# Kernel optimization log

Hardware: AMD Instinct MI355X
Metric: run time of the kernel (lower is better)

The kernel has to match this reference:

```python
import jax, jax.numpy as jnp
import numpy as np

N = 100000
E = 640000
D_IN = 128
D_OUT = 128
EPS = 0.0


def setup_inputs() -> dict:
    key = jax.random.key(0)
    k1, k2, k3, k4, k5, k6 = jax.random.split(key, 6)
    x = jax.random.normal(k1, (N, D_IN), dtype=jnp.float32)
    edge_index = jax.random.randint(k2, (2, E), 0, N, dtype=jnp.int64)
    # MLP params (Linear(in,out) -> ReLU -> Linear(out,out)), PyTorch-style init scale
    s1 = 1.0 / np.sqrt(D_IN)
    s2 = 1.0 / np.sqrt(D_OUT)
    W1 = jax.random.uniform(k3, (D_IN, D_OUT), minval=-s1, maxval=s1, dtype=jnp.float32)
    b1 = jax.random.uniform(k4, (D_OUT,), minval=-s1, maxval=s1, dtype=jnp.float32)
    W2 = jax.random.uniform(k5, (D_OUT, D_OUT), minval=-s2, maxval=s2, dtype=jnp.float32)
    b2 = jax.random.uniform(k6, (D_OUT,), minval=-s2, maxval=s2, dtype=jnp.float32)
    return {"x": x, "edge_index": edge_index, "W1": W1, "b1": b1, "W2": W2, "b2": b2}


def reference(x, edge_index, W1, b1, W2, b2):
    row, col = edge_index[0], edge_index[1]
    # gather source features, scatter-add into destination nodes
    aggregated = jax.ops.segment_sum(x[row], col, num_segments=N)  # [N, D_IN]
    h = (1.0 + EPS) * x + aggregated
    h = jnp.maximum(h @ W1 + b1, 0.0)
    return h @ W2 + b2
```

## Files before the change

kernel.cpp:

```cpp
#include <hip/hip_runtime.h>

#define NN 100000
#define EE 640000
#define DD 128

#define CVT_BLKS  12500
#define PREP_BLKS 128
#define ZERO_BLKS 98

typedef short bf16x8 __attribute__((ext_vector_type(8)));
typedef float f32x4 __attribute__((ext_vector_type(4)));

__device__ __forceinline__ unsigned short f2bf(float f) {
    union { float f; unsigned int u; } a; a.f = f;
    unsigned int u = a.u + 0x7fffu + ((a.u >> 16) & 1u);
    return (unsigned short)(u >> 16);
}

__device__ __forceinline__ int wave_incl_scan(int v, int lane) {
#pragma unroll
    for (int d = 1; d < 64; d <<= 1) {
        int u = __shfl_up(v, d, 64);
        if (lane >= d) v += u;
    }
    return v;
}

__global__ __launch_bounds__(256) void k_setup(const float* __restrict__ x,
                                               const float* __restrict__ W1,
                                               const float* __restrict__ W2,
                                               unsigned short* __restrict__ xb,
                                               unsigned short* __restrict__ w1t,
                                               unsigned short* __restrict__ w2t,
                                               int* __restrict__ cnt) {
    int b = blockIdx.x, t = threadIdx.x;
    if (b < CVT_BLKS) {
        int i = (b * 256 + t) * 4;
        float4 v = *reinterpret_cast<const float4*>(x + i);
        unsigned int u0 = (unsigned)f2bf(v.x) | ((unsigned)f2bf(v.y) << 16);
        unsigned int u1 = (unsigned)f2bf(v.z) | ((unsigned)f2bf(v.w) << 16);
        *reinterpret_cast<uint2*>(xb + i) = make_uint2(u0, u1);
    } else if (b < CVT_BLKS + PREP_BLKS) {
        int idx = (b - CVT_BLKS) * 256 + t;
        const float* W = (idx < DD * DD) ? W1 : W2;
        unsigned short* O = (idx < DD * DD) ? w1t : w2t;
        int i = idx & (DD * DD - 1);
        int n = i >> 7, k = i & (DD - 1);
        O[i] = f2bf(W[k * DD + n]);
    } else {
        int idx = (b - CVT_BLKS - PREP_BLKS) * 256 + t;
        if (idx < 25001)
            reinterpret_cast<int4*>(cnt)[idx] = make_int4(0, 0, 0, 0);
    }
}

__global__ __launch_bounds__(256) void k_hist(const int* __restrict__ ei,
                                              int* __restrict__ cnt) {
    int e = blockIdx.x * 256 + threadIdx.x;
    if (e >= EE) return;
    atomicAdd(&cnt[ei[EE + e]], 1);
}

__global__ __launch_bounds__(256) void k_offs(int* __restrict__ cnt,
                                              int* __restrict__ offs,
                                              int* __restrict__ gcount) {
    int t = threadIdx.x, lane = t & 63, w = t >> 6;
    int i = blockIdx.x * 256 + t;
    int v = (i < NN) ? cnt[i] : 0;
    int s = wave_incl_scan(v, lane);
    __shared__ int wsum[4];
    __shared__ int base;
    if (lane == 63) wsum[w] = s;
    __syncthreads();
    if (t == 0)
        base = atomicAdd(gcount, wsum[0] + wsum[1] + wsum[2] + wsum[3]);
    __syncthreads();
    int off = base;
    for (int k = 0; k < w; ++k) off += wsum[k];
    int start = off + s - v;
    if (i < NN) { offs[i] = start; cnt[i] = start; }
}

__global__ __launch_bounds__(256) void k_fill(const int* __restrict__ ei,
                                              int* __restrict__ cnt,
                                              int* __restrict__ bucket) {
    int e = blockIdx.x * 256 + threadIdx.x;
    if (e >= EE) return;
    int r = ei[e];
    int c = ei[EE + e];
    int p = atomicAdd(&cnt[c], 1);
    bucket[p] = r;
}

__global__ __launch_bounds__(256) void k_gather(const unsigned int* __restrict__ xr,
                                                const int* __restrict__ offs,
                                                const int* __restrict__ cnt,
                                                const int* __restrict__ bucket,
                                                unsigned int* __restrict__ hb) {
    int gid = blockIdx.x * 256 + threadIdx.x;
    int n = gid >> 6;
    if (n >= NN) return;
    int l = gid & 63;
    unsigned int u = xr[(size_t)n * 64 + l];
    float ax = __uint_as_float(u << 16);
    float ay = __uint_as_float(u & 0xffff0000u);
    int j = offs[n], je = cnt[n];
    for (; j + 7 < je; j += 8) {
        int a0 = bucket[j],     a1 = bucket[j + 1], a2 = bucket[j + 2], a3 = bucket[j + 3];
        int a4 = bucket[j + 4], a5 = bucket[j + 5], a6 = bucket[j + 6], a7 = bucket[j + 7];
        unsigned int u0 = xr[(size_t)a0 * 64 + l];
        unsigned int u1 = xr[(size_t)a1 * 64 + l];
        unsigned int u2 = xr[(size_t)a2 * 64 + l];
        unsigned int u3 = xr[(size_t)a3 * 64 + l];
        unsigned int u4 = xr[(size_t)a4 * 64 + l];
        unsigned int u5 = xr[(size_t)a5 * 64 + l];
        unsigned int u6 = xr[(size_t)a6 * 64 + l];
        unsigned int u7 = xr[(size_t)a7 * 64 + l];
        ax += __uint_as_float(u0 << 16) + __uint_as_float(u1 << 16)
            + __uint_as_float(u2 << 16) + __uint_as_float(u3 << 16)
            + __uint_as_float(u4 << 16) + __uint_as_float(u5 << 16)
            + __uint_as_float(u6 << 16) + __uint_as_float(u7 << 16);
        ay += __uint_as_float(u0 & 0xffff0000u) + __uint_as_float(u1 & 0xffff0000u)
            + __uint_as_float(u2 & 0xffff0000u) + __uint_as_float(u3 & 0xffff0000u)
            + __uint_as_float(u4 & 0xffff0000u) + __uint_as_float(u5 & 0xffff0000u)
            + __uint_as_float(u6 & 0xffff0000u) + __uint_as_float(u7 & 0xffff0000u);
    }
    if (j + 3 < je) {
        int a0 = bucket[j], a1 = bucket[j + 1], a2 = bucket[j + 2], a3 = bucket[j + 3];
        unsigned int u0 = xr[(size_t)a0 * 64 + l];
        unsigned int u1 = xr[(size_t)a1 * 64 + l];
        unsigned int u2 = xr[(size_t)a2 * 64 + l];
        unsigned int u3 = xr[(size_t)a3 * 64 + l];
        ax += __uint_as_float(u0 << 16) + __uint_as_float(u1 << 16)
            + __uint_as_float(u2 << 16) + __uint_as_float(u3 << 16);
        ay += __uint_as_float(u0 & 0xffff0000u) + __uint_as_float(u1 & 0xffff0000u)
            + __uint_as_float(u2 & 0xffff0000u) + __uint_as_float(u3 & 0xffff0000u);
        j += 4;
    }
    for (; j < je; ++j) {
        unsigned int uu = xr[(size_t)bucket[j] * 64 + l];
        ax += __uint_as_float(uu << 16);
        ay += __uint_as_float(uu & 0xffff0000u);
    }
    hb[(size_t)n * 64 + l] = (unsigned)f2bf(ax) | ((unsigned)f2bf(ay) << 16);
}

__global__ __launch_bounds__(256, 2) void k_mlp(const unsigned short* __restrict__ hb,
                                                const unsigned short* __restrict__ w1t,
                                                const unsigned short* __restrict__ w2t,
                                                const float* __restrict__ b1,
                                                const float* __restrict__ b2,
                                                float* __restrict__ out) {
    __shared__ unsigned short lds[DD * DD];
    const int t  = threadIdx.x;
    const int w  = t >> 6, l = t & 63;
    const int wr = w >> 1, wc = w & 1;
    const int hi = l >> 4, lo = l & 15;
    const long base_row = (long)blockIdx.x * 128;

    const uint4* hrow = reinterpret_cast<const uint4*>(hb);
#pragma unroll
    for (int it = 0; it < 8; ++it) {
        int idx = it * 256 + t;
        int row = idx >> 4;
        long g = base_row + row;
        uint4 v = make_uint4(0u, 0u, 0u, 0u);
        if (g < NN) v = hrow[base_row * 16 + idx];
        int byte = (row * 256 + (idx & 15) * 16) ^ ((row & 7) << 4);
        *reinterpret_cast<uint4*>(reinterpret_cast<char*>(lds) + byte) = v;
    }
    __syncthreads();

    const f32x4 zero = {0.f, 0.f, 0.f, 0.f};

    bf16x8 bw1[4][4];
#pragma unroll
    for (int n = 0; n < 4; ++n)
#pragma unroll
        for (int k = 0; k < 4; ++k)
            bw1[n][k] = *reinterpret_cast<const bf16x8*>(
                w1t + (wc * 64 + n * 16 + lo) * DD + k * 32 + hi * 8);

    f32x4 acc[4][4];
#pragma unroll
    for (int m = 0; m < 4; ++m)
#pragma unroll
        for (int n = 0; n < 4; ++n) acc[m][n] = zero;
#pragma unroll
    for (int m = 0; m < 4; ++m) {
        bf16x8 a[4];
        int r = wr * 64 + m * 16 + lo;
#pragma unroll
        for (int k = 0; k < 4; ++k) {
            int byte = (r * 256 + k * 64 + hi * 16) ^ ((r & 7) << 4);
            a[k] = *reinterpret_cast<const bf16x8*>(reinterpret_cast<const char*>(lds) + byte);
        }
#pragma unroll
        for (int n = 0; n < 4; ++n)
#pragma unroll
            for (int k = 0; k < 4; ++k)
                acc[m][n] = __builtin_amdgcn_mfma_f32_16x16x32_bf16(a[k], bw1[n][k], acc[m][n], 0, 0, 0);
    }
    __syncthreads();

    float bias1[4];
#pragma unroll
    for (int n = 0; n < 4; ++n) bias1[n] = b1[wc * 64 + n * 16 + lo];
#pragma unroll
    for (int m = 0; m < 4; ++m)
#pragma unroll
        for (int n = 0; n < 4; ++n)
#pragma unroll
            for (int g = 0; g < 4; ++g) {
                int row = wr * 64 + m * 16 + hi * 4 + g;
                int col = wc * 64 + n * 16 + lo;
                float v = fmaxf(acc[m][n][g] + bias1[n], 0.f);
                int byte = (row * 256 + col * 2) ^ ((row & 7) << 4);
                *reinterpret_cast<unsigned short*>(reinterpret_cast<char*>(lds) + byte) = f2bf(v);
            }
    __syncthreads();

    bf16x8 bw2[4][4];
#pragma unroll
    for (int n = 0; n < 4; ++n)
#pragma unroll
        for (int k = 0; k < 4; ++k)
            bw2[n][k] = *reinterpret_cast<const bf16x8*>(
                w2t + (wc * 64 + n * 16 + lo) * DD + k * 32 + hi * 8);

    f32x4 acc2[4][4];
#pragma unroll
    for (int m = 0; m < 4; ++m)
#pragma unroll
        for (int n = 0; n < 4; ++n) acc2[m][n] = zero;
#pragma unroll
    for (int m = 0; m < 4; ++m) {
        bf16x8 a[4];
        int r = wr * 64 + m * 16 + lo;
#pragma unroll
        for (int k = 0; k < 4; ++k) {
            int byte = (r * 256 + k * 64 + hi * 16) ^ ((r & 7) << 4);
            a[k] = *reinterpret_cast<const bf16x8*>(reinterpret_cast<const char*>(lds) + byte);
        }
#pragma unroll
        for (int n = 0; n < 4; ++n)
#pragma unroll
            for (int k = 0; k < 4; ++k)
                acc2[m][n] = __builtin_amdgcn_mfma_f32_16x16x32_bf16(a[k], bw2[n][k], acc2[m][n], 0, 0, 0);
    }

    float bias2[4];
#pragma unroll
    for (int n = 0; n < 4; ++n) bias2[n] = b2[wc * 64 + n * 16 + lo];
#pragma unroll
    for (int m = 0; m < 4; ++m)
#pragma unroll
        for (int n = 0; n < 4; ++n)
#pragma unroll
            for (int g = 0; g < 4; ++g) {
                long row = base_row + wr * 64 + m * 16 + hi * 4 + g;
                if (row < NN)
                    out[row * DD + wc * 64 + n * 16 + lo] = acc2[m][n][g] + bias2[n];
            }
}

extern "C" void kernel_launch(void* const* d_in, const int* in_sizes, int n_in,
                              void* d_out, int out_size, void* d_ws, size_t ws_size,
                              hipStream_t stream) {
    const float* x  = (const float*)d_in[0];
    const int*   ei = (const int*)d_in[1];
    const float* W1 = (const float*)d_in[2];
    const float* b1 = (const float*)d_in[3];
    const float* W2 = (const float*)d_in[4];
    const float* b2 = (const float*)d_in[5];
    float* out = (float*)d_out;

    char* ws = (char*)d_ws;
    unsigned short* xb  = (unsigned short*)ws;
    unsigned short* w1t = (unsigned short*)(ws + 25600000);
    unsigned short* w2t = w1t + DD * DD;
    unsigned short* hb  = (unsigned short*)(ws + 25665536);
    int* cnt    = (int*)(ws + 51265536);
    int* offs   = cnt + NN + 4;
    int* bucket = offs + NN + 4;

    k_setup<<<CVT_BLKS + PREP_BLKS + ZERO_BLKS, 256, 0, stream>>>(x, W1, W2, xb, w1t, w2t, cnt);
    k_hist<<<(EE + 255) / 256, 256, 0, stream>>>(ei, cnt);
    k_offs<<<(NN + 255) / 256, 256, 0, stream>>>(cnt, offs, cnt + NN);
    k_fill<<<(EE + 255) / 256, 256, 0, stream>>>(ei, cnt, bucket);
    k_gather<<<(NN * 64 + 255) / 256, 256, 0, stream>>>(
        (const unsigned int*)xb, offs, cnt, bucket, (unsigned int*)hb);
    k_mlp<<<(NN + 127) / 128, 256, 0, stream>>>(hb, w1t, w2t, b1, b2, out);
}
```

Measured before the change: 253.5 us.

## Fuse all stages into one persistent cooperative kernel with grid syncs

Replaces six separate kernel launches with a single cooperative persistent kernel that runs zeroing, histogram, conversion, scan, bucket fill, gather and MLP as phases separated by grid.sync. Grid-stride loops replace per-stage grids, and the host queries occupancy and CU count to size the grid. The aim is to remove launch gaps between the small stages. In exchange, every phase runs at the register and LDS occupancy of the heaviest MFMA phase, and grid-wide barriers add their own cost.

Measured after the change: 660.0 us. +160.3%, slower.

```diff
diff --git a/kernel.cpp b/kernel.cpp
--- a/kernel.cpp
+++ b/kernel.cpp
@@ -1,12 +1,11 @@
 #include <hip/hip_runtime.h>
+#include <hip/hip_cooperative_groups.h>
+
+namespace cg = cooperative_groups;
 
 #define NN 100000
 #define EE 640000
 #define DD 128
-
-#define CVT_BLKS  12500
-#define PREP_BLKS 128
-#define ZERO_BLKS 98
 
 typedef short bf16x8 __attribute__((ext_vector_type(8)));
 typedef float f32x4 __attribute__((ext_vector_type(4)));
@@ -26,242 +25,236 @@
     return v;
 }
 
-__global__ __launch_bounds__(256) void k_setup(const float* __restrict__ x,
-                                               const float* __restrict__ W1,
-                                               const float* __restrict__ W2,
-                                               unsigned short* __restrict__ xb,
-                                               unsigned short* __restrict__ w1t,
-                                               unsigned short* __restrict__ w2t,
-                                               int* __restrict__ cnt) {
-    int b = blockIdx.x, t = threadIdx.x;
-    if (b < CVT_BLKS) {
-        int i = (b * 256 + t) * 4;
-        float4 v = *reinterpret_cast<const float4*>(x + i);
+__global__ __launch_bounds__(256, 4) void k_mega(
+    const float* __restrict__ x, const int* __restrict__ ei,
+    const float* __restrict__ W1, const float* __restrict__ b1,
+    const float* __restrict__ W2, const float* __restrict__ b2,
+    float* __restrict__ out,
+    unsigned short* __restrict__ xb, unsigned short* __restrict__ w1t,
+    unsigned short* __restrict__ w2t, unsigned short* __restrict__ hb,
+    int* __restrict__ cnt, int* __restrict__ offs, int* __restrict__ bucket)
+{
+    cg::grid_group grid = cg::this_grid();
+    const int t = threadIdx.x;
+    const int bid = blockIdx.x;
+    const int nb = gridDim.x;
+    const int gthreads = nb * 256;
+    const int gt = bid * 256 + t;
+    const int lane = t & 63, wv = t >> 6;
+
+    __shared__ unsigned short lds[DD * DD];
+    __shared__ int wsum[4];
+    __shared__ int base;
+
+    for (int i = gt; i < (NN + 4) / 4; i += gthreads)
+        reinterpret_cast<int4*>(cnt)[i] = make_int4(0, 0, 0, 0);
+    grid.sync();
+
+    for (int e = gt; e < EE; e += gthreads)
+        atomicAdd(&cnt[ei[EE + e]], 1);
+    for (int i = gt; i < NN * DD / 4; i += gthreads) {
+        float4 v = *reinterpret_cast<const float4*>(x + (size_t)i * 4);
         unsigned int u0 = (unsigned)f2bf(v.x) | ((unsigned)f2bf(v.y) << 16);
         unsigned int u1 = (unsigned)f2bf(v.z) | ((unsigned)f2bf(v.w) << 16);
-        *reinterpret_cast<uint2*>(xb + i) = make_uint2(u0, u1);
-    } else if (b < CVT_BLKS + PREP_BLKS) {
-        int idx = (b - CVT_BLKS) * 256 + t;
+        *reinterpret_cast<uint2*>(xb + (size_t)i * 4) = make_uint2(u0, u1);
+    }
+    for (int idx = gt; idx < 2 * DD * DD; idx += gthreads) {
         const float* W = (idx < DD * DD) ? W1 : W2;
         unsigned short* O = (idx < DD * DD) ? w1t : w2t;
         int i = idx & (DD * DD - 1);
         int n = i >> 7, k = i & (DD - 1);
         O[i] = f2bf(W[k * DD + n]);
-    } else {
-        int idx = (b - CVT_BLKS - PREP_BLKS) * 256 + t;
-        if (idx < 25001)
-            reinterpret_cast<int4*>(cnt)[idx] = make_int4(0, 0, 0, 0);
-    }
-}
-
-__global__ __launch_bounds__(256) void k_hist(const int* __restrict__ ei,
-                                              int* __restrict__ cnt) {
-    int e = blockIdx.x * 256 + threadIdx.x;
-    if (e >= EE) return;
-    atomicAdd(&cnt[ei[EE + e]], 1);
-}
-
-__global__ __launch_bounds__(256) void k_offs(int* __restrict__ cnt,
-                                              int* __restrict__ offs,
-                                              int* __restrict__ gcount) {
-    int t = threadIdx.x, lane = t & 63, w = t >> 6;
-    int i = blockIdx.x * 256 + t;
-    int v = (i < NN) ? cnt[i] : 0;
-    int s = wave_incl_scan(v, lane);
-    __shared__ int wsum[4];
-    __shared__ int base;
-    if (lane == 63) wsum[w] = s;
-    __syncthreads();
-    if (t == 0)
-        base = atomicAdd(gcount, wsum[0] + wsum[1] + wsum[2] + wsum[3]);
-    __syncthreads();
-    int off = base;
-    for (int k = 0; k < w; ++k) off += wsum[k];
-    int start = off + s - v;
-    if (i < NN) { offs[i] = start; cnt[i] = start; }
-}
-
-__global__ __launch_bounds__(256) void k_fill(const int* __restrict__ ei,
-                                              int* __restrict__ cnt,
-                                              int* __restrict__ bucket) {
-    int e = blockIdx.x * 256 + threadIdx.x;
-    if (e >= EE) return;
-    int r = ei[e];
-    int c = ei[EE + e];
-    int p = atomicAdd(&cnt[c], 1);
-    bucket[p] = r;
-}
-
-__global__ __launch_bounds__(256) void k_gather(const unsigned int* __restrict__ xr,
-                                                const int* __restrict__ offs,
-                                                const int* __restrict__ cnt,
-                                                const int* __restrict__ bucket,
-                                                unsigned int* __restrict__ hb) {
-    int gid = blockIdx.x * 256 + threadIdx.x;
-    int n = gid >> 6;
-    if (n >= NN) return;
-    int l = gid & 63;
-    unsigned int u = xr[(size_t)n * 64 + l];
-    float ax = __uint_as_float(u << 16);
-    float ay = __uint_as_float(u & 0xffff0000u);
-    int j = offs[n], je = cnt[n];
-    for (; j + 7 < je; j += 8) {
-        int a0 = bucket[j],     a1 = bucket[j + 1], a2 = bucket[j + 2], a3 = bucket[j + 3];
-        int a4 = bucket[j + 4], a5 = bucket[j + 5], a6 = bucket[j + 6], a7 = bucket[j + 7];
-        unsigned int u0 = xr[(size_t)a0 * 64 + l];
-        unsigned int u1 = xr[(size_t)a1 * 64 + l];
-        unsigned int u2 = xr[(size_t)a2 * 64 + l];
-        unsigned int u3 = xr[(size_t)a3 * 64 + l];
-        unsigned int u4 = xr[(size_t)a4 * 64 + l];
-        unsigned int u5 = xr[(size_t)a5 * 64 + l];
-        unsigned int u6 = xr[(size_t)a6 * 64 + l];
-        unsigned int u7 = xr[(size_t)a7 * 64 + l];
-        ax += __uint_as_float(u0 << 16) + __uint_as_float(u1 << 16)
-            + __uint_as_float(u2 << 16) + __uint_as_float(u3 << 16)
-            + __uint_as_float(u4 << 16) + __uint_as_float(u5 << 16)
-            + __uint_as_float(u6 << 16) + __uint_as_float(u7 << 16);
-        ay += __uint_as_float(u0 & 0xffff0000u) + __uint_as_float(u1 & 0xffff0000u)
-            + __uint_as_float(u2 & 0xffff0000u) + __uint_as_float(u3 & 0xffff0000u)
-            + __uint_as_float(u4 & 0xffff0000u) + __uint_as_float(u5 & 0xffff0000u)
-            + __uint_as_float(u6 & 0xffff0000u) + __uint_as_float(u7 & 0xffff0000u);
-    }
-    if (j + 3 < je) {
-        int a0 = bucket[j], a1 = bucket[j + 1], a2 = bucket[j + 2], a3 = bucket[j + 3];
-        unsigned int u0 = xr[(size_t)a0 * 64 + l];
-        unsigned int u1 = xr[(size_t)a1 * 64 + l];
-        unsigned int u2 = xr[(size_t)a2 * 64 + l];
-        unsigned int u3 = xr[(size_t)a3 * 64 + l];
-        ax += __uint_as_float(u0 << 16) + __uint_as_float(u1 << 16)
-            + __uint_as_float(u2 << 16) + __uint_as_float(u3 << 16);
-        ay += __uint_as_float(u0 & 0xffff0000u) + __uint_as_float(u1 & 0xffff0000u)
-            + __uint_as_float(u2 & 0xffff0000u) + __uint_as_float(u3 & 0xffff0000u);
-        j += 4;
-    }
-    for (; j < je; ++j) {
-        unsigned int uu = xr[(size_t)bucket[j] * 64 + l];
-        ax += __uint_as_float(uu << 16);
-        ay += __uint_as_float(uu & 0xffff0000u);
-    }
-    hb[(size_t)n * 64 + l] = (unsigned)f2bf(ax) | ((unsigned)f2bf(ay) << 16);
-}
-
-__global__ __launch_bounds__(256, 2) void k_mlp(const unsigned short* __restrict__ hb,
-                                                const unsigned short* __restrict__ w1t,
-                                                const unsigned short* __restrict__ w2t,
-                                                const float* __restrict__ b1,
-                                                const float* __restrict__ b2,
-                                                float* __restrict__ out) {
-    __shared__ unsigned short lds[DD * DD];
-    const int t  = threadIdx.x;
-    const int w  = t >> 6, l = t & 63;
-    const int wr = w >> 1, wc = w & 1;
-    const int hi = l >> 4, lo = l & 15;
-    const long base_row = (long)blockIdx.x * 128;
-
-    const uint4* hrow = reinterpret_cast<const uint4*>(hb);
-#pragma unroll
-    for (int it = 0; it < 8; ++it) {
-        int idx = it * 256 + t;
-        int row = idx >> 4;
-        long g = base_row + row;
-        uint4 v = make_uint4(0u, 0u, 0u, 0u);
-        if (g < NN) v = hrow[base_row * 16 + idx];
-        int byte = (row * 256 + (idx & 15) * 16) ^ ((row & 7) << 4);
-        *reinterpret_cast<uint4*>(reinterpret_cast<char*>(lds) + byte) = v;
-    }
-    __syncthreads();
-
-    const f32x4 zero = {0.f, 0.f, 0.f, 0.f};
-
-    bf16x8 bw1[4][4];
-#pragma unroll
-    for (int n = 0; n < 4; ++n)
-#pragma unroll
-        for (int k = 0; k < 4; ++k)
-            bw1[n][k] = *reinterpret_cast<const bf16x8*>(
-                w1t + (wc * 64 + n * 16 + lo) * DD + k * 32 + hi * 8);
-
-    f32x4 acc[4][4];
-#pragma unroll
-    for (int m = 0; m < 4; ++m)
-#pragma unroll
-        for (int n = 0; n < 4; ++n) acc[m][n] = zero;
-#pragma unroll
-    for (int m = 0; m < 4; ++m) {
-        bf16x8 a[4];
-        int r = wr * 64 + m * 16 + lo;
-#pragma unroll
-        for (int k = 0; k < 4; ++k) {
-            int byte = (r * 256 + k * 64 + hi * 16) ^ ((r & 7) << 4);
-            a[k] = *reinterpret_cast<const bf16x8*>(reinterpret_cast<const char*>(lds) + byte);
+    }
+    grid.sync();
+
+    for (int tile = bid; tile < (NN + 255) / 256; tile += nb) {
+        int i = tile * 256 + t;
+        int v = (i < NN) ? cnt[i] : 0;
+        int s = wave_incl_scan(v, lane);
+        if (lane == 63) wsum[wv] = s;
+        __syncthreads();
+        if (t == 0)
+            base = atomicAdd(&cnt[NN], wsum[0] + wsum[1] + wsum[2] + wsum[3]);
+        __syncthreads();
+        int off = base;
+        for (int k = 0; k < wv; ++k) off += wsum[k];
+        int start = off + s - v;
+        if (i < NN) { offs[i] = start; cnt[i] = start; }
+        __syncthreads();
+    }
+    grid.sync();
+
+    for (int e = gt; e < EE; e += gthreads) {
+        int r = ei[e];
+        int c = ei[EE + e];
+        bucket[atomicAdd(&cnt[c], 1)] = r;
+    }
+    grid.sync();
+
+    {
+        const unsigned int* xr = reinterpret_cast<const unsigned int*>(xb);
+        unsigned int* hbw = reinterpret_cast<unsigned int*>(hb);
+        int gw = bid * 4 + wv, nw = nb * 4;
+        for (int n = gw; n < NN; n += nw) {
+            unsigned int u = xr[(size_t)n * 64 + lane];
+            float ax = __uint_as_float(u << 16);
+            float ay = __uint_as_float(u & 0xffff0000u);
+            int j = offs[n], je = cnt[n];
+            for (; j + 7 < je; j += 8) {
+                int a0 = bucket[j],     a1 = bucket[j + 1], a2 = bucket[j + 2], a3 = bucket[j + 3];
+                int a4 = bucket[j + 4], a5 = bucket[j + 5], a6 = bucket[j + 6], a7 = bucket[j + 7];
+                unsigned int u0 = xr[(size_t)a0 * 64 + lane];
+                unsigned int u1 = xr[(size_t)a1 * 64 + lane];
+                unsigned int u2 = xr[(size_t)a2 * 64 + lane];
+                unsigned int u3 = xr[(size_t)a3 * 64 + lane];
+                unsigned int u4 = xr[(size_t)a4 * 64 + lane];
+                unsigned int u5 = xr[(size_t)a5 * 64 + lane];
+                unsigned int u6 = xr[(size_t)a6 * 64 + lane];
+                unsigned int u7 = xr[(size_t)a7 * 64 + lane];
+                ax += __uint_as_float(u0 << 16) + __uint_as_float(u1 << 16)
+                    + __uint_as_float(u2 << 16) + __uint_as_float(u3 << 16)
+                    + __uint_as_float(u4 << 16) + __uint_as_float(u5 << 16)
+                    + __uint_as_float(u6 << 16) + __uint_as_float(u7 << 16);
+                ay += __uint_as_float(u0 & 0xffff0000u) + __uint_as_float(u1 & 0xffff0000u)
+                    + __uint_as_float(u2 & 0xffff0000u) + __uint_as_float(u3 & 0xffff0000u)
+                    + __uint_as_float(u4 & 0xffff0000u) + __uint_as_float(u5 & 0xffff0000u)
+                    + __uint_as_float(u6 & 0xffff0000u) + __uint_as_float(u7 & 0xffff0000u);
+            }
+            if (j + 3 < je) {
+                int a0 = bucket[j], a1 = bucket[j + 1], a2 = bucket[j + 2], a3 = bucket[j + 3];
+                unsigned int u0 = xr[(size_t)a0 * 64 + lane];
+                unsigned int u1 = xr[(size_t)a1 * 64 + lane];
+                unsigned int u2 = xr[(size_t)a2 * 64 + lane];
+                unsigned int u3 = xr[(size_t)a3 * 64 + lane];
+                ax += __uint_as_float(u0 << 16) + __uint_as_float(u1 << 16)
+                    + __uint_as_float(u2 << 16) + __uint_as_float(u3 << 16);
+                ay += __uint_as_float(u0 & 0xffff0000u) + __uint_as_float(u1 & 0xffff0000u)
+                    + __uint_as_float(u2 & 0xffff0000u) + __uint_as_float(u3 & 0xffff0000u);
+                j += 4;
+            }
+            for (; j < je; ++j) {
+                unsigned int uu = xr[(size_t)bucket[j] * 64 + lane];
+                ax += __uint_as_float(uu << 16);
+                ay += __uint_as_float(uu & 0xffff0000u);
+            }
+            hbw[(size_t)n * 64 + lane] = (unsigned)f2bf(ax) | ((unsigned)f2bf(ay) << 16);
         }
-#pragma unroll
-        for (int n = 0; n < 4; ++n)
-#pragma unroll
-            for (int k = 0; k < 4; ++k)
-                acc[m][n] = __builtin_amdgcn_mfma_f32_16x16x32_bf16(a[k], bw1[n][k], acc[m][n], 0, 0, 0);
-    }
-    __syncthreads();
-
-    float bias1[4];
-#pragma unroll
-    for (int n = 0; n < 4; ++n) bias1[n] = b1[wc * 64 + n * 16 + lo];
-#pragma unroll
-    for (int m = 0; m < 4; ++m)
-#pragma unroll
-        for (int n = 0; n < 4; ++n)
-#pragma unroll
-            for (int g = 0; g < 4; ++g) {
-                int row = wr * 64 + m * 16 + hi * 4 + g;
-                int col = wc * 64 + n * 16 + lo;
-                float v = fmaxf(acc[m][n][g] + bias1[n], 0.f);
-                int byte = (row * 256 + col * 2) ^ ((row & 7) << 4);
-                *reinterpret_cast<unsigned short*>(reinterpret_cast<char*>(lds) + byte) = f2bf(v);
-            }
-    __syncthreads();
-
-    bf16x8 bw2[4][4];
-#pragma unroll
-    for (int n = 0; n < 4; ++n)
-#pragma unroll
-        for (int k = 0; k < 4; ++k)
-            bw2[n][k] = *reinterpret_cast<const bf16x8*>(
-                w2t + (wc * 64 + n * 16 + lo) * DD + k * 32 + hi * 8);
-
-    f32x4 acc2[4][4];
-#pragma unroll
-    for (int m = 0; m < 4; ++m)
-#pragma unroll
-        for (int n = 0; n < 4; ++n) acc2[m][n] = zero;
-#pragma unroll
-    for (int m = 0; m < 4; ++m) {
-        bf16x8 a[4];
-        int r = wr * 64 + m * 16 + lo;
-#pragma unroll
-        for (int k = 0; k < 4; ++k) {
-            int byte = (r * 256 + k * 64 + hi * 16) ^ ((r & 7) << 4);
-            a[k] = *reinterpret_cast<const bf16x8*>(reinterpret_cast<const char*>(lds) + byte);
+    }
+    grid.sync();
+
+    {
+        const int wr = wv >> 1, wc = wv & 1;
+        const int hi = lane >> 4, lo = lane & 15;
+        const f32x4 zero = {0.f, 0.f, 0.f, 0.f};
+        const uint4* hrow = reinterpret_cast<const uint4*>(hb);
+
+        for (int tile = bid; tile < (NN + 127) / 128; tile += nb) {
+            const long base_row = (long)tile * 128;
+
+#pragma unroll
+            for (int it = 0; it < 8; ++it) {
+                int idx = it * 256 + t;
+                int row = idx >> 4;
+                long g = base_row + row;
+                uint4 v = make_uint4(0u, 0u, 0u, 0u);
+                if (g < NN) v = hrow[base_row * 16 + idx];
+                int byte = (row * 256 + (idx & 15) * 16) ^ ((row & 7) << 4);
+                *reinterpret_cast<uint4*>(reinterpret_cast<char*>(lds) + byte) = v;
+            }
+            __syncthreads();
+
+            bf16x8 bw1[4][4];
+#pragma unroll
+            for (int n = 0; n < 4; ++n)
+#pragma unroll
+                for (int k = 0; k < 4; ++k)
+                    bw1[n][k] = *reinterpret_cast<const bf16x8*>(
+                        w1t + (wc * 64 + n * 16 + lo) * DD + k * 32 + hi * 8);
+
+            f32x4 acc[4][4];
+#pragma unroll
+            for (int m = 0; m < 4; ++m)
+#pragma unroll
+                for (int n = 0; n < 4; ++n) acc[m][n] = zero;
+#pragma unroll
+            for (int m = 0; m < 4; ++m) {
+                bf16x8 a[4];
+                int r = wr * 64 + m * 16 + lo;
+#pragma unroll
+                for (int k = 0; k < 4; ++k) {
+                    int byte = (r * 256 + k * 64 + hi * 16) ^ ((r & 7) << 4);
+                    a[k] = *reinterpret_cast<const bf16x8*>(reinterpret_cast<const char*>(lds) + byte);
+                }
+#pragma unroll
+                for (int n = 0; n < 4; ++n)
+#pragma unroll
+                    for (int k = 0; k < 4; ++k)
+                        acc[m][n] = __builtin_amdgcn_mfma_f32_16x16x32_bf16(a[k], bw1[n][k], acc[m][n], 0, 0, 0);
+            }
+            __syncthreads();
+
+            float bias1[4];
+#pragma unroll
+            for (int n = 0; n < 4; ++n) bias1[n] = b1[wc * 64 + n * 16 + lo];
+#pragma unroll
+            for (int m = 0; m < 4; ++m)
+#pragma unroll
+                for (int n = 0; n < 4; ++n)
+#pragma unroll
+                    for (int g = 0; g < 4; ++g) {
+                        int row = wr * 64 + m * 16 + hi * 4 + g;
+                        int col = wc * 64 + n * 16 + lo;
+                        float v = fmaxf(acc[m][n][g] + bias1[n], 0.f);
+                        int byte = (row * 256 + col * 2) ^ ((row & 7) << 4);
+                        *reinterpret_cast<unsigned short*>(reinterpret_cast<char*>(lds) + byte) = f2bf(v);
+                    }
+            __syncthreads();
+
+            bf16x8 bw2[4][4];
+#pragma unroll
+            for (int n = 0; n < 4; ++n)
+#pragma unroll
+                for (int k = 0; k < 4; ++k)
+                    bw2[n][k] = *reinterpret_cast<const bf16x8*>(
+                        w2t + (wc * 64 + n * 16 + lo) * DD + k * 32 + hi * 8);
+
+            f32x4 acc2[4][4];
+#pragma unroll
+            for (int m = 0; m < 4; ++m)
+#pragma unroll
+                for (int n = 0; n < 4; ++n) acc2[m][n] = zero;
+#pragma unroll
+            for (int m = 0; m < 4; ++m) {
+                bf16x8 a[4];
+                int r = wr * 64 + m * 16 + lo;
+#pragma unroll
+                for (int k = 0; k < 4; ++k) {
+                    int byte = (r * 256 + k * 64 + hi * 16) ^ ((r & 7) << 4);
+                    a[k] = *reinterpret_cast<const bf16x8*>(reinterpret_cast<const char*>(lds) + byte);
+                }
+#pragma unroll
+                for (int n = 0; n < 4; ++n)
+#pragma unroll
+                    for (int k = 0; k < 4; ++k)
+                        acc2[m][n] = __builtin_amdgcn_mfma_f32_16x16x32_bf16(a[k], bw2[n][k], acc2[m][n], 0, 0, 0);
+            }
+
+            float bias2[4];
+#pragma unroll
+            for (int n = 0; n < 4; ++n) bias2[n] = b2[wc * 64 + n * 16 + lo];
+#pragma unroll
+            for (int m = 0; m < 4; ++m)
+#pragma unroll
+                for (int n = 0; n < 4; ++n)
+#pragma unroll
+                    for (int g = 0; g < 4; ++g) {
+                        long row = base_row + wr * 64 + m * 16 + hi * 4 + g;
+                        if (row < NN)
+                            out[row * DD + wc * 64 + n * 16 + lo] = acc2[m][n][g] + bias2[n];
+                    }
+            __syncthreads();
         }
-#pragma unroll
-        for (int n = 0; n < 4; ++n)
-#pragma unroll
-            for (int k = 0; k < 4; ++k)
-                acc2[m][n] = __builtin_amdgcn_mfma_f32_16x16x32_bf16(a[k], bw2[n][k], acc2[m][n], 0, 0, 0);
-    }
-
-    float bias2[4];
-#pragma unroll
-    for (int n = 0; n < 4; ++n) bias2[n] = b2[wc * 64 + n * 16 + lo];
-#pragma unroll
-    for (int m = 0; m < 4; ++m)
-#pragma unroll
-        for (int n = 0; n < 4; ++n)
-#pragma unroll
-            for (int g = 0; g < 4; ++g) {
-                long row = base_row + wr * 64 + m * 16 + hi * 4 + g;
-                if (row < NN)
-                    out[row * DD + wc * 64 + n * 16 + lo] = acc2[m][n][g] + bias2[n];
-            }
+    }
 }
 
 extern "C" void kernel_launch(void* const* d_in, const int* in_sizes, int n_in,
@@ -284,11 +277,18 @@
     int* offs   = cnt + NN + 4;
     int* bucket = offs + NN + 4;
 
-    k_setup<<<CVT_BLKS + PREP_BLKS + ZERO_BLKS, 256, 0, stream>>>(x, W1, W2, xb, w1t, w2t, cnt);
-    k_hist<<<(EE + 255) / 256, 256, 0, stream>>>(ei, cnt);
-    k_offs<<<(NN + 255) / 256, 256, 0, stream>>>(cnt, offs, cnt + NN);
-    k_fill<<<(EE + 255) / 256, 256, 0, stream>>>(ei, cnt, bucket);
-    k_gather<<<(NN * 64 + 255) / 256, 256, 0, stream>>>(
-        (const unsigned int*)xb, offs, cnt, bucket, (unsigned int*)hb);
-    k_mlp<<<(NN + 127) / 128, 256, 0, stream>>>(hb, w1t, w2t, b1, b2, out);
-}
+    int occ = 0;
+    hipOccupancyMaxActiveBlocksPerMultiprocessor(&occ, (const void*)k_mega, 256, 0);
+    if (occ < 1) occ = 1;
+    if (occ > 4) occ = 4;
+    int dev = 0, cus = 0;
+    hipGetDevice(&dev);
+    hipDeviceGetAttribute(&cus, hipDeviceAttributeMultiprocessorCount, dev);
+    if (cus <= 0) cus = 256;
+    int grid = occ * cus;
+
+    void* args[] = {(void*)&x, (void*)&ei, (void*)&W1, (void*)&b1, (void*)&W2, (void*)&b2,
+                    (void*)&out, (void*)&xb, (void*)&w1t, (void*)&w2t, (void*)&hb,
+                    (void*)&cnt, (void*)&offs, (void*)&bucket};
+    hipLaunchCooperativeKernel((const void*)k_mega, dim3(grid), dim3(256), args, 0, stream);
+}
```

## Fuse setup with histogram and record per-edge slots to drop fill atomics

Applied to the files above, without the earlier changes.

Merges the bf16 conversion, weight transpose and destination histogram into one grid-stride kernel, where the atomicAdd return value is stored as each edge's slot within its destination bucket. The fill kernel then places edges at offs[c]+slot without a second pass of atomics, and k_offs writes end offsets directly. The count zeroing moves to a memset and one kernel launch is removed. The cost is an extra 2.5MB slot array that must be written and read back.

Measured after the change: 226.3 us. 10.7% less time.

```diff
diff --git a/kernel.cpp b/kernel.cpp
--- a/kernel.cpp
+++ b/kernel.cpp
@@ -3,10 +3,6 @@
 #define NN 100000
 #define EE 640000
 #define DD 128
-
-#define CVT_BLKS  12500
-#define PREP_BLKS 128
-#define ZERO_BLKS 98
 
 typedef short bf16x8 __attribute__((ext_vector_type(8)));
 typedef float f32x4 __attribute__((ext_vector_type(4)));
@@ -26,70 +22,65 @@
     return v;
 }
 
-__global__ __launch_bounds__(256) void k_setup(const float* __restrict__ x,
-                                               const float* __restrict__ W1,
-                                               const float* __restrict__ W2,
-                                               unsigned short* __restrict__ xb,
-                                               unsigned short* __restrict__ w1t,
-                                               unsigned short* __restrict__ w2t,
-                                               int* __restrict__ cnt) {
-    int b = blockIdx.x, t = threadIdx.x;
-    if (b < CVT_BLKS) {
-        int i = (b * 256 + t) * 4;
-        float4 v = *reinterpret_cast<const float4*>(x + i);
+__global__ __launch_bounds__(256) void k_su_hist(const float* __restrict__ x,
+                                                 const float* __restrict__ W1,
+                                                 const float* __restrict__ W2,
+                                                 const int* __restrict__ ei,
+                                                 unsigned short* __restrict__ xb,
+                                                 unsigned short* __restrict__ w1t,
+                                                 unsigned short* __restrict__ w2t,
+                                                 int* __restrict__ cnt,
+                                                 int* __restrict__ eslot) {
+    const int gt = blockIdx.x * 256 + threadIdx.x;
+    const int gthreads = gridDim.x * 256;
+    for (int i = gt; i < NN * DD / 4; i += gthreads) {
+        float4 v = *reinterpret_cast<const float4*>(x + (size_t)i * 4);
         unsigned int u0 = (unsigned)f2bf(v.x) | ((unsigned)f2bf(v.y) << 16);
         unsigned int u1 = (unsigned)f2bf(v.z) | ((unsigned)f2bf(v.w) << 16);
-        *reinterpret_cast<uint2*>(xb + i) = make_uint2(u0, u1);
-    } else if (b < CVT_BLKS + PREP_BLKS) {
-        int idx = (b - CVT_BLKS) * 256 + t;
+        *reinterpret_cast<uint2*>(xb + (size_t)i * 4) = make_uint2(u0, u1);
+    }
+    for (int idx = gt; idx < 2 * DD * DD; idx += gthreads) {
         const float* W = (idx < DD * DD) ? W1 : W2;
         unsigned short* O = (idx < DD * DD) ? w1t : w2t;
         int i = idx & (DD * DD - 1);
         int n = i >> 7, k = i & (DD - 1);
         O[i] = f2bf(W[k * DD + n]);
-    } else {
-        int idx = (b - CVT_BLKS - PREP_BLKS) * 256 + t;
-        if (idx < 25001)
-            reinterpret_cast<int4*>(cnt)[idx] = make_int4(0, 0, 0, 0);
-    }
-}
-
-__global__ __launch_bounds__(256) void k_hist(const int* __restrict__ ei,
-                                              int* __restrict__ cnt) {
-    int e = blockIdx.x * 256 + threadIdx.x;
-    if (e >= EE) return;
-    atomicAdd(&cnt[ei[EE + e]], 1);
+    }
+    for (int e = gt; e < EE; e += gthreads) {
+        int c = ei[EE + e];
+        eslot[e] = atomicAdd(&cnt[c], 1);
+    }
 }
 
 __global__ __launch_bounds__(256) void k_offs(int* __restrict__ cnt,
                                               int* __restrict__ offs,
                                               int* __restrict__ gcount) {
-    int t = threadIdx.x, lane = t & 63, w = t >> 6;
+    int t = threadIdx.x, lane = t & 63, wv = t >> 6;
     int i = blockIdx.x * 256 + t;
     int v = (i < NN) ? cnt[i] : 0;
     int s = wave_incl_scan(v, lane);
     __shared__ int wsum[4];
     __shared__ int base;
-    if (lane == 63) wsum[w] = s;
+    if (lane == 63) wsum[wv] = s;
     __syncthreads();
     if (t == 0)
         base = atomicAdd(gcount, wsum[0] + wsum[1] + wsum[2] + wsum[3]);
     __syncthreads();
     int off = base;
-    for (int k = 0; k < w; ++k) off += wsum[k];
+    for (int k = 0; k < wv; ++k) off += wsum[k];
     int start = off + s - v;
-    if (i < NN) { offs[i] = start; cnt[i] = start; }
+    if (i < NN) { offs[i] = start; cnt[i] = start + v; }
 }
 
 __global__ __launch_bounds__(256) void k_fill(const int* __restrict__ ei,
-                                              int* __restrict__ cnt,
+                                              const int* __restrict__ eslot,
+                                              const int* __restrict__ offs,
                                               int* __restrict__ bucket) {
     int e = blockIdx.x * 256 + threadIdx.x;
     if (e >= EE) return;
     int r = ei[e];
     int c = ei[EE + e];
-    int p = atomicAdd(&cnt[c], 1);
-    bucket[p] = r;
+    bucket[offs[c] + eslot[e]] = r;
 }
 
 __global__ __launch_bounds__(256) void k_gather(const unsigned int* __restrict__ xr,
@@ -282,12 +273,13 @@
     unsigned short* hb  = (unsigned short*)(ws + 25665536);
     int* cnt    = (int*)(ws + 51265536);
     int* offs   = cnt + NN + 4;
-    int* bucket = offs + NN + 4;
-
-    k_setup<<<CVT_BLKS + PREP_BLKS + ZERO_BLKS, 256, 0, stream>>>(x, W1, W2, xb, w1t, w2t, cnt);
-    k_hist<<<(EE + 255) / 256, 256, 0, stream>>>(ei, cnt);
+    int* eslot  = offs + NN + 4;
+    int* bucket = eslot + EE;
+
+    hipMemsetAsync(cnt, 0, (NN + 4) * sizeof(int), stream);
+    k_su_hist<<<3200, 256, 0, stream>>>(x, W1, W2, ei, xb, w1t, w2t, cnt, eslot);
     k_offs<<<(NN + 255) / 256, 256, 0, stream>>>(cnt, offs, cnt + NN);
-    k_fill<<<(EE + 255) / 256, 256, 0, stream>>>(ei, cnt, bucket);
+    k_fill<<<(EE + 255) / 256, 256, 0, stream>>>(ei, eslot, offs, bucket);
     k_gather<<<(NN * 64 + 255) / 256, 256, 0, stream>>>(
         (const unsigned int*)xb, offs, cnt, bucket, (unsigned int*)hb);
     k_mlp<<<(NN + 127) / 128, 256, 0, stream>>>(hb, w1t, w2t, b1, b2, out);
```
